# Kernel tuning notes

Measured on AMD Instinct MI355X. Metric: run time of the kernel, lower is better.

## Reference

```python
import jax, jax.numpy as jnp
import numpy as np

HEADS = 8

def setup_inputs() -> dict:
    key = jax.random.key(0)
    ks = jax.random.split(key, 6)
    B, S, C = 32, 1024, 640  # B = n_videos(2) * video_length(16)
    s = 1.0 / np.sqrt(C)
    return {
        "hidden_states": jax.random.normal(ks[0], (B, S, C), jnp.float32),
        "Wq": jax.random.normal(ks[1], (C, C), jnp.float32) * s,
        "Wk": jax.random.normal(ks[2], (C, C), jnp.float32) * s,
        "Wv": jax.random.normal(ks[3], (C, C), jnp.float32) * s,
        "Wo": jax.random.normal(ks[4], (C, C), jnp.float32) * s,
        "bq": jnp.zeros((C,), jnp.float32),
        "bk": jnp.zeros((C,), jnp.float32),
        "bv": jnp.zeros((C,), jnp.float32),
        "bo": jnp.zeros((C,), jnp.float32),
        "video_length": 16,
    }

def reference(hidden_states, Wq, Wk, Wv, Wo, bq, bk, bv, bo, video_length):
    B, S, C = hidden_states.shape
    f = video_length
    b = B // f
    H = HEADS
    D = C // H
    residual = hidden_states

    # Query from all frames
    q = hidden_states @ Wq + bq                      # [B, S, C]
    # K/V computed ONLY from frame 0 of each video (sparse-causal sharing)
    x0 = hidden_states.reshape(b, f, S, C)[:, 0]     # [b, S, C]
    k = x0 @ Wk + bk                                 # [b, S, C]
    v = x0 @ Wv + bv                                 # [b, S, C]

    q = q.reshape(b, f, S, H, D).transpose(0, 1, 3, 2, 4)  # [b, f, H, S, D]
    k = k.reshape(b, S, H, D).transpose(0, 2, 1, 3)        # [b, H, S, D]
    v = v.reshape(b, S, H, D).transpose(0, 2, 1, 3)        # [b, H, S, D]

    scale = 1.0 / np.sqrt(D)
    scores = jnp.einsum('bfhsd,bhtd->bfhst', q, k) * scale  # [b, f, H, S, S]
    probs = jax.nn.softmax(scores, axis=-1)
    out = jnp.einsum('bfhst,bhtd->bfhsd', probs, v)          # [b, f, H, S, D]

    out = out.transpose(0, 1, 3, 2, 4).reshape(B, S, C)
    out = out @ Wo + bo
    return out + residual
```

## Files before the change

### kernel.cpp

```cpp
#include <hip/hip_runtime.h>
#include <math.h>

#define C_DIM 640
#define S_DIM 1024
#define H_NUM 8
#define D_DIM 80
#define FRAMES 16

typedef __attribute__((ext_vector_type(8))) short short8;
typedef __attribute__((ext_vector_type(4))) float f32x4;
typedef unsigned short ushort_t;

__device__ __forceinline__ ushort_t f2bf(float x) {
    union { float f; unsigned u; } uf; uf.f = x;
    unsigned r = uf.u + 0x7fffu + ((uf.u >> 16) & 1u);
    return (ushort_t)(r >> 16);
}

__global__ __launch_bounds__(256)
void conv_bf16(const float* __restrict__ in, ushort_t* __restrict__ out, int n8) {
    int i = blockIdx.x * 256 + threadIdx.x;
    if (i >= n8) return;
    const float4* p = (const float4*)(in + (long long)i * 8);
    float4 a = p[0], b = p[1];
    short8 o;
    o[0] = (short)f2bf(a.x); o[1] = (short)f2bf(a.y);
    o[2] = (short)f2bf(a.z); o[3] = (short)f2bf(a.w);
    o[4] = (short)f2bf(b.x); o[5] = (short)f2bf(b.y);
    o[6] = (short)f2bf(b.z); o[7] = (short)f2bf(b.w);
    *(short8*)(out + (long long)i * 8) = o;
}

__global__ __launch_bounds__(256)
void transpose_w(const float* __restrict__ W, ushort_t* __restrict__ T) {
    __shared__ float Ls[64][65];
    const int tid = threadIdx.x;
    const int r0 = blockIdx.y * 64, c0 = blockIdx.x * 64;
    for (int e = tid; e < 4096; e += 256) {
        int r = e >> 6, c = e & 63;
        Ls[c][r] = W[(long long)(r0 + r) * C_DIM + c0 + c];
    }
    __syncthreads();
    for (int e = tid; e < 4096; e += 256) {
        int cc = e >> 6, rr = e & 63;
        T[(long long)(c0 + cc) * C_DIM + r0 + rr] = f2bf(Ls[cc][rr]);
    }
}

__global__ __launch_bounds__(256)
void gemm_bf16(const ushort_t* __restrict__ A, const ushort_t* __restrict__ Wt,
               const float* __restrict__ bias, const float* __restrict__ residual,
               void* __restrict__ outp, int out_bf16, float out_scale,
               int nTilesN, int rpg_shift, long long a_gs)
{
    __shared__ ushort_t As[128 * 40];
    __shared__ ushort_t Bs[128 * 40];

    const int tid = threadIdx.x, bid = blockIdx.x;
    const int bm = bid / nTilesN, bn = bid % nTilesN;
    const int m0 = bm * 128, n0 = bn * 128;
    const int w = tid >> 6, l = tid & 63, g = l >> 4, li = l & 15;

    const int r0c = tid >> 2, cc = (tid & 3) * 8;
    const int maskR = (1 << rpg_shift) - 1;
    const int rowA0 = m0 + r0c, rowA1 = rowA0 + 64;
    const ushort_t* aP0 = A + (long long)(rowA0 >> rpg_shift) * a_gs
                            + (long long)(rowA0 & maskR) * C_DIM + cc;
    const ushort_t* aP1 = A + (long long)(rowA1 >> rpg_shift) * a_gs
                            + (long long)(rowA1 & maskR) * C_DIM + cc;
    const ushort_t* bP0 = Wt + (long long)(n0 + r0c) * C_DIM + cc;
    const ushort_t* bP1 = bP0 + 64 * C_DIM;
    const int sIdx0 = r0c * 40 + cc, sIdx1 = sIdx0 + 64 * 40;

    f32x4 acc[2][8] = {};

    for (int k0 = 0; k0 < C_DIM; k0 += 32) {
        __syncthreads();
        *(short8*)&As[sIdx0] = *(const short8*)(aP0 + k0);
        *(short8*)&As[sIdx1] = *(const short8*)(aP1 + k0);
        *(short8*)&Bs[sIdx0] = *(const short8*)(bP0 + k0);
        *(short8*)&Bs[sIdx1] = *(const short8*)(bP1 + k0);
        __syncthreads();
        short8 av0 = *(const short8*)&As[(32 * w + li) * 40 + 8 * g];
        short8 av1 = *(const short8*)&As[(32 * w + 16 + li) * 40 + 8 * g];
        #pragma unroll
        for (int cf = 0; cf < 8; ++cf) {
            short8 bv = *(const short8*)&Bs[(16 * cf + li) * 40 + 8 * g];
            acc[0][cf] = __builtin_amdgcn_mfma_f32_16x16x32_bf16(av0, bv, acc[0][cf], 0, 0, 0);
            acc[1][cf] = __builtin_amdgcn_mfma_f32_16x16x32_bf16(av1, bv, acc[1][cf], 0, 0, 0);
        }
    }

    #pragma unroll
    for (int fr = 0; fr < 2; ++fr) {
        #pragma unroll
        for (int cf = 0; cf < 8; ++cf) {
            const int col = n0 + 16 * cf + li;
            const float bcol = bias[col];
            #pragma unroll
            for (int r = 0; r < 4; ++r) {
                const int row = m0 + 32 * w + 16 * fr + 4 * g + r;
                float vv = (acc[fr][cf][r] + bcol) * out_scale;
                if (residual) vv += residual[(long long)row * C_DIM + col];
                if (out_bf16) ((ushort_t*)outp)[(long long)row * C_DIM + col] = f2bf(vv);
                else          ((float*)outp)[(long long)row * C_DIM + col] = vv;
            }
        }
    }
}

__global__ __launch_bounds__(256)
void attn_mfma(const ushort_t* __restrict__ Qb, const ushort_t* __restrict__ Kb,
               const ushort_t* __restrict__ Vb, ushort_t* __restrict__ Ob)
{
    __shared__ ushort_t Qs[64 * 88];
    __shared__ ushort_t Ks[64 * 88];
    __shared__ ushort_t Vt[80 * 64];
    __shared__ ushort_t Ps[64 * 64];

    const int tid = threadIdx.x, bid = blockIdx.x;
    const int sb = bid & 15, f = (bid >> 4) & 15, h = (bid >> 8) & 7, v = bid >> 11;
    const int s0 = sb * 64;
    const int w = tid >> 6, l = tid & 63, g = l >> 4, li = l & 15;

    const ushort_t* Qg = Qb + (long long)((v * FRAMES + f) * S_DIM + s0) * C_DIM + h * D_DIM;
    const ushort_t* Kg = Kb + (long long)v * S_DIM * C_DIM + h * D_DIM;
    const ushort_t* Vg = Vb + (long long)v * S_DIM * C_DIM + h * D_DIM;

    for (int e = tid; e < 640; e += 256) {
        int t = e / 10, c = e - 10 * t;
        *(short8*)&Qs[t * 88 + c * 8] = *(const short8*)(Qg + t * C_DIM + c * 8);
    }

    float m_run[4], l_run[4];
    #pragma unroll
    for (int r = 0; r < 4; ++r) { m_run[r] = -1e30f; l_run[r] = 0.f; }
    f32x4 accv[5] = {};
    __syncthreads();

    for (int t0 = 0; t0 < S_DIM; t0 += 64) {
        for (int e = tid; e < 640; e += 256) {
            int t = e / 10, c = e - 10 * t;
            *(short8*)&Ks[t * 88 + c * 8] = *(const short8*)(Kg + (t0 + t) * C_DIM + c * 8);
            short8 v8 = *(const short8*)(Vg + (t0 + t) * C_DIM + c * 8);
            int d0 = c * 8;
            #pragma unroll
            for (int j = 0; j < 8; ++j)
                Vt[((d0 + j) * 64 + t) ^ (j << 3)] = (ushort_t)v8[j];
        }
        __syncthreads();

        f32x4 sc[4] = {};
        #pragma unroll
        for (int ks = 0; ks < 3; ++ks) {
            const bool valid = (ks < 2) || (g < 2);
            short8 aq = {};
            if (valid) aq = *(const short8*)&Qs[(16 * w + li) * 88 + ks * 32 + 8 * g];
            #pragma unroll
            for (int tf = 0; tf < 4; ++tf) {
                short8 bk = {};
                if (valid) bk = *(const short8*)&Ks[(16 * tf + li) * 88 + ks * 32 + 8 * g];
                sc[tf] = __builtin_amdgcn_mfma_f32_16x16x32_bf16(aq, bk, sc[tf], 0, 0, 0);
            }
        }

        float mt[4];
        #pragma unroll
        for (int r = 0; r < 4; ++r)
            mt[r] = fmaxf(fmaxf(sc[0][r], sc[1][r]), fmaxf(sc[2][r], sc[3][r]));
        #pragma unroll
        for (int mk = 1; mk < 16; mk <<= 1)
            #pragma unroll
            for (int r = 0; r < 4; ++r)
                mt[r] = fmaxf(mt[r], __shfl_xor(mt[r], mk, 64));
        float sca[4];
        #pragma unroll
        for (int r = 0; r < 4; ++r) {
            float mn = fmaxf(m_run[r], mt[r]);
            sca[r] = __expf(m_run[r] - mn);
            m_run[r] = mn;
        }
        float ps[4] = {0.f, 0.f, 0.f, 0.f};
        #pragma unroll
        for (int tf = 0; tf < 4; ++tf) {
            #pragma unroll
            for (int r = 0; r < 4; ++r) {
                float p = __expf(sc[tf][r] - m_run[r]);
                ps[r] += p;
                const int q = 16 * w + 4 * g + r;
                Ps[(q * 64 + 16 * tf + li) ^ (((4 * g + r) & 7) << 3)] = f2bf(p);
            }
        }
        #pragma unroll
        for (int mk = 1; mk < 16; mk <<= 1)
            #pragma unroll
            for (int r = 0; r < 4; ++r)
                ps[r] += __shfl_xor(ps[r], mk, 64);
        #pragma unroll
        for (int r = 0; r < 4; ++r) l_run[r] = l_run[r] * sca[r] + ps[r];
        #pragma unroll
        for (int df = 0; df < 5; ++df)
            #pragma unroll
            for (int r = 0; r < 4; ++r) accv[df][r] *= sca[r];

        __syncthreads();

        #pragma unroll
        for (int ks = 0; ks < 2; ++ks) {
            short8 pa = *(const short8*)&Ps[((16 * w + li) * 64 + ks * 32 + 8 * g) ^ ((li & 7) << 3)];
            #pragma unroll
            for (int df = 0; df < 5; ++df) {
                short8 vb = *(const short8*)&Vt[((16 * df + li) * 64 + ks * 32 + 8 * g) ^ ((li & 7) << 3)];
                accv[df] = __builtin_amdgcn_mfma_f32_16x16x32_bf16(pa, vb, accv[df], 0, 0, 0);
            }
        }
        __syncthreads();
    }

    const long long obase = (long long)((v * FRAMES + f) * S_DIM + s0) * C_DIM + h * D_DIM;
    float inv[4];
    #pragma unroll
    for (int r = 0; r < 4; ++r) inv[r] = 1.0f / l_run[r];
    #pragma unroll
    for (int df = 0; df < 5; ++df)
        #pragma unroll
        for (int r = 0; r < 4; ++r)
            Ob[obase + (long long)(16 * w + 4 * g + r) * C_DIM + 16 * df + li] =
                f2bf(accv[df][r] * inv[r]);
}

extern "C" void kernel_launch(void* const* d_in, const int* in_sizes, int n_in,
                              void* d_out, int out_size, void* d_ws, size_t ws_size,
                              hipStream_t stream) {
    const float* hs = (const float*)d_in[0];
    const float* Wq = (const float*)d_in[1];
    const float* Wk = (const float*)d_in[2];
    const float* Wv = (const float*)d_in[3];
    const float* Wo = (const float*)d_in[4];
    const float* bq = (const float*)d_in[5];
    const float* bk = (const float*)d_in[6];
    const float* bv = (const float*)d_in[7];
    const float* bo = (const float*)d_in[8];
    float* out = (float*)d_out;

    ushort_t* ws = (ushort_t*)d_ws;
    ushort_t* hsbf = ws;
    ushort_t* Wtq  = hsbf + 32768LL * 640;
    ushort_t* Wtk  = Wtq + 640LL * 640;
    ushort_t* Wtv  = Wtk + 640LL * 640;
    ushort_t* Wto  = Wtv + 640LL * 640;
    ushort_t* Qbf  = Wto + 640LL * 640;
    ushort_t* Kbf  = Qbf + 32768LL * 640;
    ushort_t* Vbf  = Kbf + 2048LL * 640;
    ushort_t* Obf  = Vbf + 2048LL * 640;

    dim3 blk(256);
    const float scale = 0.11180339887498948f;
    const long long hs_gs = 16LL * S_DIM * C_DIM;

    conv_bf16<<<10240, blk, 0, stream>>>(hs, hsbf, 32768 * 640 / 8);
    transpose_w<<<dim3(10, 10), blk, 0, stream>>>(Wq, Wtq);
    transpose_w<<<dim3(10, 10), blk, 0, stream>>>(Wk, Wtk);
    transpose_w<<<dim3(10, 10), blk, 0, stream>>>(Wv, Wtv);
    transpose_w<<<dim3(10, 10), blk, 0, stream>>>(Wo, Wto);

    gemm_bf16<<<(32768 / 128) * 5, blk, 0, stream>>>(
        hsbf, Wtq, bq, nullptr, Qbf, 1, scale, 5, 15, 0LL);
    gemm_bf16<<<(2048 / 128) * 5, blk, 0, stream>>>(
        hsbf, Wtk, bk, nullptr, Kbf, 1, 1.0f, 5, 10, hs_gs);
    gemm_bf16<<<(2048 / 128) * 5, blk, 0, stream>>>(
        hsbf, Wtv, bv, nullptr, Vbf, 1, 1.0f, 5, 10, hs_gs);

    attn_mfma<<<2 * H_NUM * FRAMES * (S_DIM / 64), blk, 0, stream>>>(Qbf, Kbf, Vbf, Obf);

    gemm_bf16<<<(32768 / 128) * 5, blk, 0, stream>>>(
        Obf, Wto, bo, hs, out, 0, 1.0f, 5, 15, 0LL);
}
```

Measured before the change: 800.0 us.

## Write V pre-transposed from projection GEMM and use exp2 softmax

```diff
diff --git a/kernel.cpp b/kernel.cpp
--- a/kernel.cpp
+++ b/kernel.cpp
@@ -8,6 +8,7 @@
 #define FRAMES 16
 
 typedef __attribute__((ext_vector_type(8))) short short8;
+typedef __attribute__((ext_vector_type(4))) short short4v;
 typedef __attribute__((ext_vector_type(4))) float f32x4;
 typedef unsigned short ushort_t;
 
@@ -50,7 +51,7 @@
 __global__ __launch_bounds__(256)
 void gemm_bf16(const ushort_t* __restrict__ A, const ushort_t* __restrict__ Wt,
                const float* __restrict__ bias, const float* __restrict__ residual,
-               void* __restrict__ outp, int out_bf16, float out_scale,
+               void* __restrict__ outp, int out_mode, float out_scale,
                int nTilesN, int rpg_shift, long long a_gs)
 {
     __shared__ ushort_t As[128 * 40];
@@ -97,13 +98,27 @@
         for (int cf = 0; cf < 8; ++cf) {
             const int col = n0 + 16 * cf + li;
             const float bcol = bias[col];
-            #pragma unroll
-            for (int r = 0; r < 4; ++r) {
-                const int row = m0 + 32 * w + 16 * fr + 4 * g + r;
-                float vv = (acc[fr][cf][r] + bcol) * out_scale;
-                if (residual) vv += residual[(long long)row * C_DIM + col];
-                if (out_bf16) ((ushort_t*)outp)[(long long)row * C_DIM + col] = f2bf(vv);
-                else          ((float*)outp)[(long long)row * C_DIM + col] = vv;
+            if (out_mode == 2) {
+                const int h = col / 80, dd = col - h * 80;
+                const int row0 = m0 + 32 * w + 16 * fr + 4 * g;
+                const int vv = row0 >> 10, t0 = row0 & 1023;
+                short4v o;
+                #pragma unroll
+                for (int r = 0; r < 4; ++r)
+                    o[r] = (short)f2bf(acc[fr][cf][r] + bcol);
+                *(short4v*)((ushort_t*)outp +
+                    ((long long)(vv * 8 + h) * 80 + dd) * 1024 + t0) = o;
+            } else {
+                #pragma unroll
+                for (int r = 0; r < 4; ++r) {
+                    const int row = m0 + 32 * w + 16 * fr + 4 * g + r;
+                    float vv = (acc[fr][cf][r] + bcol) * out_scale;
+                    if (residual) vv += residual[(long long)row * C_DIM + col];
+                    if (out_mode == 1)
+                        ((ushort_t*)outp)[(long long)row * C_DIM + col] = f2bf(vv);
+                    else
+                        ((float*)outp)[(long long)row * C_DIM + col] = vv;
+                }
             }
         }
     }
@@ -111,12 +126,12 @@
 
 __global__ __launch_bounds__(256)
 void attn_mfma(const ushort_t* __restrict__ Qb, const ushort_t* __restrict__ Kb,
-               const ushort_t* __restrict__ Vb, ushort_t* __restrict__ Ob)
+               const ushort_t* __restrict__ VTb, ushort_t* __restrict__ Ob)
 {
-    __shared__ ushort_t Qs[64 * 88];
-    __shared__ ushort_t Ks[64 * 88];
+    __shared__ ushort_t Qs[64 * 80];
+    __shared__ ushort_t Ks[64 * 80];
     __shared__ ushort_t Vt[80 * 64];
-    __shared__ ushort_t Ps[64 * 64];
+    __shared__ ushort_t Ps[64 * 72];
 
     const int tid = threadIdx.x, bid = blockIdx.x;
     const int sb = bid & 15, f = (bid >> 4) & 15, h = (bid >> 8) & 7, v = bid >> 11;
@@ -125,11 +140,11 @@
 
     const ushort_t* Qg = Qb + (long long)((v * FRAMES + f) * S_DIM + s0) * C_DIM + h * D_DIM;
     const ushort_t* Kg = Kb + (long long)v * S_DIM * C_DIM + h * D_DIM;
-    const ushort_t* Vg = Vb + (long long)v * S_DIM * C_DIM + h * D_DIM;
+    const ushort_t* VTg = VTb + (long long)(v * H_NUM + h) * D_DIM * S_DIM;
 
     for (int e = tid; e < 640; e += 256) {
         int t = e / 10, c = e - 10 * t;
-        *(short8*)&Qs[t * 88 + c * 8] = *(const short8*)(Qg + t * C_DIM + c * 8);
+        *(short8*)&Qs[t * 80 + c * 8] = *(const short8*)(Qg + t * C_DIM + c * 8);
     }
 
     float m_run[4], l_run[4];
@@ -141,12 +156,12 @@
     for (int t0 = 0; t0 < S_DIM; t0 += 64) {
         for (int e = tid; e < 640; e += 256) {
             int t = e / 10, c = e - 10 * t;
-            *(short8*)&Ks[t * 88 + c * 8] = *(const short8*)(Kg + (t0 + t) * C_DIM + c * 8);
-            short8 v8 = *(const short8*)(Vg + (t0 + t) * C_DIM + c * 8);
-            int d0 = c * 8;
-            #pragma unroll
-            for (int j = 0; j < 8; ++j)
-                Vt[((d0 + j) * 64 + t) ^ (j << 3)] = (ushort_t)v8[j];
+            *(short8*)&Ks[t * 80 + c * 8] = *(const short8*)(Kg + (t0 + t) * C_DIM + c * 8);
+        }
+        for (int e = tid; e < 640; e += 256) {
+            int d = e >> 3, c = e & 7;
+            short8 vv = *(const short8*)(VTg + (long long)d * S_DIM + t0 + 8 * c);
+            *(short8*)&Vt[(d * 64 + 8 * c) ^ ((d & 7) << 3)] = vv;
         }
         __syncthreads();
 
@@ -155,11 +170,11 @@
         for (int ks = 0; ks < 3; ++ks) {
             const bool valid = (ks < 2) || (g < 2);
             short8 aq = {};
-            if (valid) aq = *(const short8*)&Qs[(16 * w + li) * 88 + ks * 32 + 8 * g];
+            if (valid) aq = *(const short8*)&Qs[(16 * w + li) * 80 + ks * 32 + 8 * g];
             #pragma unroll
             for (int tf = 0; tf < 4; ++tf) {
                 short8 bk = {};
-                if (valid) bk = *(const short8*)&Ks[(16 * tf + li) * 88 + ks * 32 + 8 * g];
+                if (valid) bk = *(const short8*)&Ks[(16 * tf + li) * 80 + ks * 32 + 8 * g];
                 sc[tf] = __builtin_amdgcn_mfma_f32_16x16x32_bf16(aq, bk, sc[tf], 0, 0, 0);
             }
         }
@@ -177,18 +192,19 @@
         #pragma unroll
         for (int r = 0; r < 4; ++r) {
             float mn = fmaxf(m_run[r], mt[r]);
-            sca[r] = __expf(m_run[r] - mn);
+            sca[r] = exp2f(m_run[r] - mn);
             m_run[r] = mn;
         }
         float ps[4] = {0.f, 0.f, 0.f, 0.f};
+        const int qswz = (g >> 1) << 3;
         #pragma unroll
         for (int tf = 0; tf < 4; ++tf) {
             #pragma unroll
             for (int r = 0; r < 4; ++r) {
-                float p = __expf(sc[tf][r] - m_run[r]);
+                float p = exp2f(sc[tf][r] - m_run[r]);
                 ps[r] += p;
                 const int q = 16 * w + 4 * g + r;
-                Ps[(q * 64 + 16 * tf + li) ^ (((4 * g + r) & 7) << 3)] = f2bf(p);
+                Ps[q * 72 + ((16 * tf + li) ^ qswz)] = f2bf(p);
             }
         }
         #pragma unroll
@@ -205,12 +221,13 @@
 
         __syncthreads();
 
+        const int rswz = ((li >> 3) & 1) << 3;
         #pragma unroll
         for (int ks = 0; ks < 2; ++ks) {
-            short8 pa = *(const short8*)&Ps[((16 * w + li) * 64 + ks * 32 + 8 * g) ^ ((li & 7) << 3)];
+            short8 pa = *(const short8*)&Ps[(16 * w + li) * 72 + ((32 * ks + 8 * g) ^ rswz)];
             #pragma unroll
             for (int df = 0; df < 5; ++df) {
-                short8 vb = *(const short8*)&Vt[((16 * df + li) * 64 + ks * 32 + 8 * g) ^ ((li & 7) << 3)];
+                short8 vb = *(const short8*)&Vt[((16 * df + li) * 64 + 32 * ks + 8 * g) ^ ((li & 7) << 3)];
                 accv[df] = __builtin_amdgcn_mfma_f32_16x16x32_bf16(pa, vb, accv[df], 0, 0, 0);
             }
         }
@@ -251,11 +268,11 @@
     ushort_t* Wto  = Wtv + 640LL * 640;
     ushort_t* Qbf  = Wto + 640LL * 640;
     ushort_t* Kbf  = Qbf + 32768LL * 640;
-    ushort_t* Vbf  = Kbf + 2048LL * 640;
-    ushort_t* Obf  = Vbf + 2048LL * 640;
+    ushort_t* VTbf = Kbf + 2048LL * 640;
+    ushort_t* Obf  = VTbf + 2LL * 8 * 80 * 1024;
 
     dim3 blk(256);
-    const float scale = 0.11180339887498948f;
+    const float scale = 0.11180339887498948f * 1.4426950408889634f;
     const long long hs_gs = 16LL * S_DIM * C_DIM;
 
     conv_bf16<<<10240, blk, 0, stream>>>(hs, hsbf, 32768 * 640 / 8);
@@ -269,9 +286,9 @@
     gemm_bf16<<<(2048 / 128) * 5, blk, 0, stream>>>(
         hsbf, Wtk, bk, nullptr, Kbf, 1, 1.0f, 5, 10, hs_gs);
     gemm_bf16<<<(2048 / 128) * 5, blk, 0, stream>>>(
-        hsbf, Wtv, bv, nullptr, Vbf, 1, 1.0f, 5, 10, hs_gs);
-
-    attn_mfma<<<2 * H_NUM * FRAMES * (S_DIM / 64), blk, 0, stream>>>(Qbf, Kbf, Vbf, Obf);
+        hsbf, Wtv, bv, nullptr, VTbf, 2, 1.0f, 5, 10, hs_gs);
+
+    attn_mfma<<<2 * H_NUM * FRAMES * (S_DIM / 64), blk, 0, stream>>>(Qbf, Kbf, VTbf, Obf);
 
     gemm_bf16<<<(32768 / 128) * 5, blk, 0, stream>>>(
         Obf, Wto, bo, hs, out, 0, 1.0f, 5, 15, 0LL);
```

Result: faster. 705.9 us (-11.8%).
